# Kernel tuning notes

Measured on AMD Instinct MI355X. Metric: run time of the kernel, lower is better.

Reference implementation:

```python
import jax, jax.numpy as jnp
import numpy as np

DT = 1e-3   # time step [s] (geometry.dt)
H = 10.0    # grid spacing [m] (geometry.h)

# Staggered-grid first differences (2nd-order accurate on the staggered grid).
# Periodic wrap at the boundary via roll; the damping layer d absorbs there.

def _dplus(f, ax):
    return (jnp.roll(f, -1, axis=ax) - f) / H

def _dminus(f, ax):
    return (f - jnp.roll(f, 1, axis=ax)) / H


def setup_inputs() -> dict:
    key = jax.random.key(0)
    ks = jax.random.split(key, 9)
    B, NZ, NX = 4, 2048, 2048
    vp = 1500.0 + 2500.0 * jax.random.uniform(ks[0], (NZ, NX), jnp.float32)   # P velocity [m/s]
    vs = vp / 1.73                                                            # S velocity (Poisson solid)
    rho = 1000.0 + 1000.0 * jax.random.uniform(ks[1], (NZ, NX), jnp.float32)  # density [kg/m^3]
    fields = {}
    for i, name in enumerate(['vx', 'vz', 'txx', 'tzz', 'txz']):
        fields[name] = 1e-3 * jax.random.normal(ks[2 + i], (B, NZ, NX), jnp.float32)
    d = 50.0 * jax.random.uniform(ks[8], (NZ, NX), jnp.float32)               # PML damping profile
    return dict(vp=vp, vs=vs, rho=rho, **fields, d=d)


def reference(vp, vs, rho, vx, vz, txx, tzz, txz, d):
    # Lame parameters from (vp, vs, rho)
    mu = rho * vs * vs
    lam = rho * vp * vp - 2.0 * mu
    # Split-free damping update: y = (1-c)/(1+c) * y_old + dt/(1+c) * rhs
    c = 0.5 * DT * d            # [nz, nx], broadcasts over shot dim
    a = (1.0 - c) / (1.0 + c)
    b = DT / (1.0 + c)
    # --- velocity update (leapfrog: uses old stresses) ---
    vx_new = a * vx + b * (_dminus(txx, -1) + _dminus(txz, -2)) / rho
    vz_new = a * vz + b * (_dplus(txz, -1) + _dplus(tzz, -2)) / rho
    # --- stress update (uses new velocities) ---
    vx_x = _dplus(vx_new, -1)
    vz_z = _dminus(vz_new, -2)
    txx_new = a * txx + b * ((lam + 2.0 * mu) * vx_x + lam * vz_z)
    tzz_new = a * tzz + b * ((lam + 2.0 * mu) * vz_z + lam * vx_x)
    txz_new = a * txz + b * mu * (_dplus(vx_new, -2) + _dminus(vz_new, -1))
    # hidden state for next time step: [5, B, nz, nx]
    return jnp.stack([vx_new, vz_new, txx_new, tzz_new, txz_new])
```

## Files before the change

### kernel.cpp

```cpp
#include <hip/hip_runtime.h>


constexpr int NZ = 2048;
constexpr int NX = 2048;
constexpr int B  = 4;
constexpr int PLANE = NZ * NX;
constexpr int VOL   = B * PLANE;
constexpr float DT    = 1e-3f;
constexpr float INV_H = 0.1f;
constexpr int NBLK  = (PLANE / 4) / 256;
constexpr int NXCD  = 8;
constexpr int BLK_PER_XCD = NBLK / NXCD;

typedef float f32x4 __attribute__((ext_vector_type(4)));

__device__ __forceinline__ float rcpf(float x) { return __builtin_amdgcn_rcpf(x); }
__device__ __forceinline__ float4 ld4(const float* __restrict__ p) {
    return *reinterpret_cast<const float4*>(p);
}
__device__ __forceinline__ void st_nt4(float* __restrict__ p,
                                       float a, float b, float c, float d) {
    f32x4 v = {a, b, c, d};
    __builtin_nontemporal_store(v, reinterpret_cast<f32x4*>(p));
}

__global__ __launch_bounds__(256) void wave_fused_v4(
    const float* __restrict__ vp,  const float* __restrict__ vs,
    const float* __restrict__ rho,
    const float* __restrict__ vx,  const float* __restrict__ vz,
    const float* __restrict__ txx, const float* __restrict__ tzz,
    const float* __restrict__ txz,
    const float* __restrict__ dd,
    float* __restrict__ out)
{
    const int bid = blockIdx.x;
    const int sb  = (bid & (NXCD - 1)) * BLK_PER_XCD + (bid >> 3);
    const int t   = sb * blockDim.x + threadIdx.x;
    const int xg = (t & (NX / 4 - 1)) << 2;
    const int z  = t >> 9;
    const int zp = (z + 1) & (NZ - 1);
    const int zm = (z - 1) & (NZ - 1);
    const int xm1 = (xg - 1) & (NX - 1);
    const int xp4 = (xg + 4) & (NX - 1);
    const int rz  = z  * NX;
    const int rzp = zp * NX;
    const int rzm = zm * NX;

    float dz6[6], rz6[6];
    {
        const float4 d4 = ld4(dd + rz + xg);
        dz6[0] = dd[rz + xm1]; dz6[1] = d4.x; dz6[2] = d4.y;
        dz6[3] = d4.z;         dz6[4] = d4.w; dz6[5] = dd[rz + xp4];
        const float4 r4 = ld4(rho + rz + xg);
        rz6[0] = rho[rz + xm1]; rz6[1] = r4.x; rz6[2] = r4.y;
        rz6[3] = r4.z;          rz6[4] = r4.w; rz6[5] = rho[rz + xp4];
    }
    float avz[6], bvz[6], inv_c[4];
    #pragma unroll
    for (int j = 0; j < 6; ++j) {
        const float c   = 0.5f * DT * dz6[j];
        const float inv = rcpf(1.0f + c);
        avz[j] = (1.0f - c) * inv;
        bvz[j] = DT * INV_H * inv * rcpf(rz6[j]);
        if (j >= 1 && j <= 4) inv_c[j - 1] = inv;
    }
    float avzp[4], bvzp[4], avzm[4], bvzm[4];
    {
        const float4 dp = ld4(dd + rzp + xg), dm = ld4(dd + rzm + xg);
        const float4 rp = ld4(rho + rzp + xg), rm = ld4(rho + rzm + xg);
        const float dpa[4] = {dp.x, dp.y, dp.z, dp.w};
        const float dma[4] = {dm.x, dm.y, dm.z, dm.w};
        const float rpa[4] = {rp.x, rp.y, rp.z, rp.w};
        const float rma[4] = {rm.x, rm.y, rm.z, rm.w};
        #pragma unroll
        for (int k = 0; k < 4; ++k) {
            float c = 0.5f * DT * dpa[k];
            float inv = rcpf(1.0f + c);
            avzp[k] = (1.0f - c) * inv;
            bvzp[k] = DT * INV_H * inv * rcpf(rpa[k]);
            c = 0.5f * DT * dma[k];
            inv = rcpf(1.0f + c);
            avzm[k] = (1.0f - c) * inv;
            bvzm[k] = DT * INV_H * inv * rcpf(rma[k]);
        }
    }
    float q1[4], q2[4], q3[4], a_s[4];
    {
        const float4 vp4 = ld4(vp + rz + xg), vs4 = ld4(vs + rz + xg);
        const float vpa[4] = {vp4.x, vp4.y, vp4.z, vp4.w};
        const float vsa[4] = {vs4.x, vs4.y, vs4.z, vs4.w};
        #pragma unroll
        for (int k = 0; k < 4; ++k) {
            const float r   = rz6[k + 1];
            const float muv = r * vsa[k] * vsa[k];
            const float lam = r * vpa[k] * vpa[k] - 2.0f * muv;
            const float bsH = DT * INV_H * inv_c[k];
            q1[k] = bsH * (lam + 2.0f * muv);
            q2[k] = bsH * lam;
            q3[k] = bsH * muv;
            a_s[k] = avz[k + 1];
        }
    }

    #pragma unroll 1
    for (int b = 0; b < B; ++b) {
        const int b3  = b * PLANE;
        const int cz  = b3 + rz  + xg;
        const int czp = b3 + rzp + xg;
        const int czm = b3 + rzm + xg;

        float txxz[6], txzz[6], tzzz[5], tzzzp[5], txxzp[5];
        float txzzm[5];
        float vxz[5];
        float vzz[5];
        {
            float4 m;
            m = ld4(txx + cz);
            txxz[1] = m.x; txxz[2] = m.y; txxz[3] = m.z; txxz[4] = m.w;
            txxz[0] = txx[b3 + rz + xm1];  txxz[5] = txx[b3 + rz + xp4];
            m = ld4(txz + cz);
            txzz[1] = m.x; txzz[2] = m.y; txzz[3] = m.z; txzz[4] = m.w;
            txzz[0] = txz[b3 + rz + xm1];  txzz[5] = txz[b3 + rz + xp4];
            m = ld4(tzz + cz);
            tzzz[1] = m.x; tzzz[2] = m.y; tzzz[3] = m.z; tzzz[4] = m.w;
            tzzz[0] = tzz[b3 + rz + xm1];
            m = ld4(tzz + czp);
            tzzzp[1] = m.x; tzzzp[2] = m.y; tzzzp[3] = m.z; tzzzp[4] = m.w;
            tzzzp[0] = tzz[b3 + rzp + xm1];
            m = ld4(txx + czp);
            txxzp[1] = m.x; txxzp[2] = m.y; txxzp[3] = m.z; txxzp[4] = m.w;
            txxzp[0] = txx[b3 + rzp + xm1];
            m = ld4(txz + czm);
            txzzm[0] = m.x; txzzm[1] = m.y; txzzm[2] = m.z; txzzm[3] = m.w;
            txzzm[4] = txz[b3 + rzm + xp4];
            m = ld4(vx + cz);
            vxz[0] = m.x; vxz[1] = m.y; vxz[2] = m.z; vxz[3] = m.w;
            vxz[4] = vx[b3 + rz + xp4];
            m = ld4(vz + cz);
            vzz[1] = m.x; vzz[2] = m.y; vzz[3] = m.z; vzz[4] = m.w;
            vzz[0] = vz[b3 + rz + xm1];
        }
        const float4 tp4 = ld4(txz + czp);
        const float4 tm4 = ld4(tzz + czm);
        const float4 vxp4 = ld4(vx + czp);
        const float4 vzm4 = ld4(vz + czm);
        const float txzzp[4] = {tp4.x, tp4.y, tp4.z, tp4.w};
        const float tzzzm[4] = {tm4.x, tm4.y, tm4.z, tm4.w};
        const float vxzp[4]  = {vxp4.x, vxp4.y, vxp4.z, vxp4.w};
        const float vzzm[4]  = {vzm4.x, vzm4.y, vzm4.z, vzm4.w};

        float vxn_z[5];
        #pragma unroll
        for (int k = 0; k < 5; ++k)
            vxn_z[k] = avz[k + 1] * vxz[k]
                     + bvz[k + 1] * ((txxz[k + 1] - txxz[k])
                                   + (txzz[k + 1] - txzzm[k]));
        float vzn_z[5];
        #pragma unroll
        for (int k = 0; k < 5; ++k)
            vzn_z[k] = avz[k] * vzz[k]
                     + bvz[k] * ((txzz[k + 1] - txzz[k])
                               + (tzzzp[k] - tzzz[k]));
        float vxn_zp[4];
        #pragma unroll
        for (int k = 0; k < 4; ++k)
            vxn_zp[k] = avzp[k] * vxzp[k]
                      + bvzp[k] * ((txxzp[k + 1] - txxzp[k])
                                 + (txzzp[k] - txzz[k + 1]));
        float vzn_zm[4];
        #pragma unroll
        for (int k = 0; k < 4; ++k)
            vzn_zm[k] = avzm[k] * vzzm[k]
                      + bvzm[k] * ((txzzm[k + 1] - txzzm[k])
                                 + (tzzz[k + 1] - tzzzm[k]));

        float oxx[4], ozz[4], oxz[4];
        #pragma unroll
        for (int k = 0; k < 4; ++k) {
            const float dvx = vxn_z[k + 1] - vxn_z[k];
            const float dvz = vzn_z[k + 1] - vzn_zm[k];
            oxx[k] = a_s[k] * txxz[k + 1] + q1[k] * dvx + q2[k] * dvz;
            ozz[k] = a_s[k] * tzzz[k + 1] + q1[k] * dvz + q2[k] * dvx;
            oxz[k] = a_s[k] * txzz[k + 1]
                   + q3[k] * ((vxn_zp[k] - vxn_z[k])
                            + (vzn_z[k + 1] - vzn_z[k]));
        }

        st_nt4(out + 0 * VOL + cz, vxn_z[0], vxn_z[1], vxn_z[2], vxn_z[3]);
        st_nt4(out + 1 * VOL + cz, vzn_z[1], vzn_z[2], vzn_z[3], vzn_z[4]);
        st_nt4(out + 2 * VOL + cz, oxx[0], oxx[1], oxx[2], oxx[3]);
        st_nt4(out + 3 * VOL + cz, ozz[0], ozz[1], ozz[2], ozz[3]);
        st_nt4(out + 4 * VOL + cz, oxz[0], oxz[1], oxz[2], oxz[3]);
    }
}

extern "C" void kernel_launch(void* const* d_in, const int* in_sizes, int n_in,
                              void* d_out, int out_size, void* d_ws, size_t ws_size,
                              hipStream_t stream) {
    const float* vp  = (const float*)d_in[0];
    const float* vs  = (const float*)d_in[1];
    const float* rho = (const float*)d_in[2];
    const float* vx  = (const float*)d_in[3];
    const float* vz  = (const float*)d_in[4];
    const float* txx = (const float*)d_in[5];
    const float* tzz = (const float*)d_in[6];
    const float* txz = (const float*)d_in[7];
    const float* dd  = (const float*)d_in[8];
    float* out = (float*)d_out;

    const int threads = 256;
    const int blocks  = NBLK;
    hipLaunchKernelGGL(wave_fused_v4, dim3(blocks), dim3(threads), 0, stream,
                       vp, vs, rho, vx, vz, txx, tzz, txz, dd, out);
}
```

Baseline: 614.5 us.

## Software-pipeline shot loop: defer stores behind next shot's loads

Replaces the per-shot loop with a fully unrolled sequence in which each shot's results are kept in registers and stored only after the following shot's loads are issued. Compiler barriers fix the order of loads and stores. The goal is to keep more global loads in flight and to stop stores from serialising against subsequent loads. This holds several output vectors live at once, which raises register pressure and may cut occupancy.

```diff
diff --git a/kernel.cpp b/kernel.cpp
--- a/kernel.cpp
+++ b/kernel.cpp
@@ -23,8 +23,16 @@
     f32x4 v = {a, b, c, d};
     __builtin_nontemporal_store(v, reinterpret_cast<f32x4*>(p));
 }
-
-__global__ __launch_bounds__(256) void wave_fused_v4(
+#define MEM_ORDER() asm volatile("" ::: "memory")
+
+struct LS {
+    float txxz[6], txzz[6], tzzz[5], tzzzp[5], txxzp[5];
+    float txzzm[5], vxz[5], vzz[5];
+    float txzzp[4], tzzzm[4], vxzp[4], vzzm[4];
+};
+struct Out { f32x4 v[5]; };
+
+__global__ __launch_bounds__(256) void wave_fused_v8(
     const float* __restrict__ vp,  const float* __restrict__ vs,
     const float* __restrict__ rho,
     const float* __restrict__ vx,  const float* __restrict__ vz,
@@ -84,7 +92,7 @@
             bvzm[k] = DT * INV_H * inv * rcpf(rma[k]);
         }
     }
-    float q1[4], q2[4], q3[4], a_s[4];
+    float q1[4], q2[4], q3[4];
     {
         const float4 vp4 = ld4(vp + rz + xg), vs4 = ld4(vs + rz + xg);
         const float vpa[4] = {vp4.x, vp4.y, vp4.z, vp4.w};
@@ -98,100 +106,116 @@
             q1[k] = bsH * (lam + 2.0f * muv);
             q2[k] = bsH * lam;
             q3[k] = bsH * muv;
-            a_s[k] = avz[k + 1];
         }
     }
 
-    #pragma unroll 1
-    for (int b = 0; b < B; ++b) {
+    auto load_shot = [&](int b, LS& L) {
         const int b3  = b * PLANE;
         const int cz  = b3 + rz  + xg;
         const int czp = b3 + rzp + xg;
         const int czm = b3 + rzm + xg;
-
-        float txxz[6], txzz[6], tzzz[5], tzzzp[5], txxzp[5];
-        float txzzm[5];
-        float vxz[5];
-        float vzz[5];
-        {
-            float4 m;
-            m = ld4(txx + cz);
-            txxz[1] = m.x; txxz[2] = m.y; txxz[3] = m.z; txxz[4] = m.w;
-            txxz[0] = txx[b3 + rz + xm1];  txxz[5] = txx[b3 + rz + xp4];
-            m = ld4(txz + cz);
-            txzz[1] = m.x; txzz[2] = m.y; txzz[3] = m.z; txzz[4] = m.w;
-            txzz[0] = txz[b3 + rz + xm1];  txzz[5] = txz[b3 + rz + xp4];
-            m = ld4(tzz + cz);
-            tzzz[1] = m.x; tzzz[2] = m.y; tzzz[3] = m.z; tzzz[4] = m.w;
-            tzzz[0] = tzz[b3 + rz + xm1];
-            m = ld4(tzz + czp);
-            tzzzp[1] = m.x; tzzzp[2] = m.y; tzzzp[3] = m.z; tzzzp[4] = m.w;
-            tzzzp[0] = tzz[b3 + rzp + xm1];
-            m = ld4(txx + czp);
-            txxzp[1] = m.x; txxzp[2] = m.y; txxzp[3] = m.z; txxzp[4] = m.w;
-            txxzp[0] = txx[b3 + rzp + xm1];
-            m = ld4(txz + czm);
-            txzzm[0] = m.x; txzzm[1] = m.y; txzzm[2] = m.z; txzzm[3] = m.w;
-            txzzm[4] = txz[b3 + rzm + xp4];
-            m = ld4(vx + cz);
-            vxz[0] = m.x; vxz[1] = m.y; vxz[2] = m.z; vxz[3] = m.w;
-            vxz[4] = vx[b3 + rz + xp4];
-            m = ld4(vz + cz);
-            vzz[1] = m.x; vzz[2] = m.y; vzz[3] = m.z; vzz[4] = m.w;
-            vzz[0] = vz[b3 + rz + xm1];
-        }
-        const float4 tp4 = ld4(txz + czp);
-        const float4 tm4 = ld4(tzz + czm);
-        const float4 vxp4 = ld4(vx + czp);
-        const float4 vzm4 = ld4(vz + czm);
-        const float txzzp[4] = {tp4.x, tp4.y, tp4.z, tp4.w};
-        const float tzzzm[4] = {tm4.x, tm4.y, tm4.z, tm4.w};
-        const float vxzp[4]  = {vxp4.x, vxp4.y, vxp4.z, vxp4.w};
-        const float vzzm[4]  = {vzm4.x, vzm4.y, vzm4.z, vzm4.w};
-
+        float4 m;
+        m = ld4(txx + cz);
+        L.txxz[1] = m.x; L.txxz[2] = m.y; L.txxz[3] = m.z; L.txxz[4] = m.w;
+        L.txxz[0] = txx[b3 + rz + xm1];  L.txxz[5] = txx[b3 + rz + xp4];
+        m = ld4(txz + cz);
+        L.txzz[1] = m.x; L.txzz[2] = m.y; L.txzz[3] = m.z; L.txzz[4] = m.w;
+        L.txzz[0] = txz[b3 + rz + xm1];  L.txzz[5] = txz[b3 + rz + xp4];
+        m = ld4(tzz + cz);
+        L.tzzz[1] = m.x; L.tzzz[2] = m.y; L.tzzz[3] = m.z; L.tzzz[4] = m.w;
+        L.tzzz[0] = tzz[b3 + rz + xm1];
+        m = ld4(tzz + czp);
+        L.tzzzp[1] = m.x; L.tzzzp[2] = m.y; L.tzzzp[3] = m.z; L.tzzzp[4] = m.w;
+        L.tzzzp[0] = tzz[b3 + rzp + xm1];
+        m = ld4(txx + czp);
+        L.txxzp[1] = m.x; L.txxzp[2] = m.y; L.txxzp[3] = m.z; L.txxzp[4] = m.w;
+        L.txxzp[0] = txx[b3 + rzp + xm1];
+        m = ld4(txz + czm);
+        L.txzzm[0] = m.x; L.txzzm[1] = m.y; L.txzzm[2] = m.z; L.txzzm[3] = m.w;
+        L.txzzm[4] = txz[b3 + rzm + xp4];
+        m = ld4(vx + cz);
+        L.vxz[0] = m.x; L.vxz[1] = m.y; L.vxz[2] = m.z; L.vxz[3] = m.w;
+        L.vxz[4] = vx[b3 + rz + xp4];
+        m = ld4(vz + cz);
+        L.vzz[1] = m.x; L.vzz[2] = m.y; L.vzz[3] = m.z; L.vzz[4] = m.w;
+        L.vzz[0] = vz[b3 + rz + xm1];
+        m = ld4(txz + czp);
+        L.txzzp[0] = m.x; L.txzzp[1] = m.y; L.txzzp[2] = m.z; L.txzzp[3] = m.w;
+        m = ld4(tzz + czm);
+        L.tzzzm[0] = m.x; L.tzzzm[1] = m.y; L.tzzzm[2] = m.z; L.tzzzm[3] = m.w;
+        m = ld4(vx + czp);
+        L.vxzp[0] = m.x; L.vxzp[1] = m.y; L.vxzp[2] = m.z; L.vxzp[3] = m.w;
+        m = ld4(vz + czm);
+        L.vzzm[0] = m.x; L.vzzm[1] = m.y; L.vzzm[2] = m.z; L.vzzm[3] = m.w;
+    };
+
+    auto compute_shot = [&](const LS& L, Out& o) {
         float vxn_z[5];
         #pragma unroll
         for (int k = 0; k < 5; ++k)
-            vxn_z[k] = avz[k + 1] * vxz[k]
-                     + bvz[k + 1] * ((txxz[k + 1] - txxz[k])
-                                   + (txzz[k + 1] - txzzm[k]));
+            vxn_z[k] = avz[k + 1] * L.vxz[k]
+                     + bvz[k + 1] * ((L.txxz[k + 1] - L.txxz[k])
+                                   + (L.txzz[k + 1] - L.txzzm[k]));
         float vzn_z[5];
         #pragma unroll
         for (int k = 0; k < 5; ++k)
-            vzn_z[k] = avz[k] * vzz[k]
-                     + bvz[k] * ((txzz[k + 1] - txzz[k])
-                               + (tzzzp[k] - tzzz[k]));
+            vzn_z[k] = avz[k] * L.vzz[k]
+                     + bvz[k] * ((L.txzz[k + 1] - L.txzz[k])
+                               + (L.tzzzp[k] - L.tzzz[k]));
         float vxn_zp[4];
         #pragma unroll
         for (int k = 0; k < 4; ++k)
-            vxn_zp[k] = avzp[k] * vxzp[k]
-                      + bvzp[k] * ((txxzp[k + 1] - txxzp[k])
-                                 + (txzzp[k] - txzz[k + 1]));
+            vxn_zp[k] = avzp[k] * L.vxzp[k]
+                      + bvzp[k] * ((L.txxzp[k + 1] - L.txxzp[k])
+                                 + (L.txzzp[k] - L.txzz[k + 1]));
         float vzn_zm[4];
         #pragma unroll
         for (int k = 0; k < 4; ++k)
-            vzn_zm[k] = avzm[k] * vzzm[k]
-                      + bvzm[k] * ((txzzm[k + 1] - txzzm[k])
-                                 + (tzzz[k + 1] - tzzzm[k]));
-
+            vzn_zm[k] = avzm[k] * L.vzzm[k]
+                      + bvzm[k] * ((L.txzzm[k + 1] - L.txzzm[k])
+                                 + (L.tzzz[k + 1] - L.tzzzm[k]));
         float oxx[4], ozz[4], oxz[4];
         #pragma unroll
         for (int k = 0; k < 4; ++k) {
             const float dvx = vxn_z[k + 1] - vxn_z[k];
             const float dvz = vzn_z[k + 1] - vzn_zm[k];
-            oxx[k] = a_s[k] * txxz[k + 1] + q1[k] * dvx + q2[k] * dvz;
-            ozz[k] = a_s[k] * tzzz[k + 1] + q1[k] * dvz + q2[k] * dvx;
-            oxz[k] = a_s[k] * txzz[k + 1]
+            oxx[k] = avz[k + 1] * L.txxz[k + 1] + q1[k] * dvx + q2[k] * dvz;
+            ozz[k] = avz[k + 1] * L.tzzz[k + 1] + q1[k] * dvz + q2[k] * dvx;
+            oxz[k] = avz[k + 1] * L.txzz[k + 1]
                    + q3[k] * ((vxn_zp[k] - vxn_z[k])
                             + (vzn_z[k + 1] - vzn_z[k]));
         }
-
-        st_nt4(out + 0 * VOL + cz, vxn_z[0], vxn_z[1], vxn_z[2], vxn_z[3]);
-        st_nt4(out + 1 * VOL + cz, vzn_z[1], vzn_z[2], vzn_z[3], vzn_z[4]);
-        st_nt4(out + 2 * VOL + cz, oxx[0], oxx[1], oxx[2], oxx[3]);
-        st_nt4(out + 3 * VOL + cz, ozz[0], ozz[1], ozz[2], ozz[3]);
-        st_nt4(out + 4 * VOL + cz, oxz[0], oxz[1], oxz[2], oxz[3]);
-    }
+        o.v[0] = f32x4{vxn_z[0], vxn_z[1], vxn_z[2], vxn_z[3]};
+        o.v[1] = f32x4{vzn_z[1], vzn_z[2], vzn_z[3], vzn_z[4]};
+        o.v[2] = f32x4{oxx[0], oxx[1], oxx[2], oxx[3]};
+        o.v[3] = f32x4{ozz[0], ozz[1], ozz[2], ozz[3]};
+        o.v[4] = f32x4{oxz[0], oxz[1], oxz[2], oxz[3]};
+    };
+
+    auto store_shot = [&](const Out& o, int b) {
+        const int cz = b * PLANE + rz + xg;
+        #pragma unroll
+        for (int k = 0; k < 5; ++k)
+            __builtin_nontemporal_store(o.v[k],
+                reinterpret_cast<f32x4*>(out + k * VOL + cz));
+    };
+
+    LS L;
+    Out o0, o1, o2, o3;
+    load_shot(0, L);
+    compute_shot(L, o0);
+    load_shot(1, L);
+    compute_shot(L, o1);
+    load_shot(2, L);
+    MEM_ORDER();
+    store_shot(o0, 0);
+    compute_shot(L, o2);
+    load_shot(3, L);
+    MEM_ORDER();
+    store_shot(o1, 1);
+    compute_shot(L, o3);
+    store_shot(o2, 2);
+    store_shot(o3, 3);
 }
 
 extern "C" void kernel_launch(void* const* d_in, const int* in_sizes, int n_in,
@@ -210,6 +234,6 @@
 
     const int threads = 256;
     const int blocks  = NBLK;
-    hipLaunchKernelGGL(wave_fused_v4, dim3(blocks), dim3(threads), 0, stream,
+    hipLaunchKernelGGL(wave_fused_v8, dim3(blocks), dim3(threads), 0, stream,
                        vp, vs, rho, vx, vz, txx, tzz, txz, dd, out);
 }
```

After: 617.7 us. No clear change (+0.5%).
